# Performance work log

Measured on AMD Instinct MI355X. Metric: run time of the kernel, lower is better.

Reference implementation:

```python
import jax, jax.numpy as jnp
import numpy as np

H = 1024

def setup_inputs() -> dict:
    key = jax.random.key(0)
    k1, k2, k3, k4, k5 = jax.random.split(key, 5)
    B, T = 32, 2048
    s = 1.0 / np.sqrt(H)
    return {
        "decoder_state": jax.random.normal(k1, (B, H), dtype=jnp.float32),
        "encoder_states": jax.random.normal(k2, (B, T, H), dtype=jnp.float32),
        "Wa_w": jax.random.uniform(k3, (H, H), jnp.float32, -s, s),
        "Wa_b": jnp.zeros((H,), jnp.float32),
        "Ua_w": jax.random.uniform(k4, (H, H), jnp.float32, -s, s),
        "Ua_b": jnp.zeros((H,), jnp.float32),
        "v_w": jax.random.uniform(k5, (H,), jnp.float32, -s, s),
        "v_b": jnp.zeros((), jnp.float32),
    }

def reference(decoder_state, encoder_states, Wa_w, Wa_b, Ua_w, Ua_b, v_w, v_b):
    # decoder_state: [B,H], encoder_states: [B,T,H]
    dec_proj = decoder_state @ Ua_w.T + Ua_b            # [B,H]
    enc_proj = jnp.einsum('bth,oh->bto', encoder_states, Wa_w) + Wa_b  # [B,T,H]
    e = jnp.tanh(dec_proj[:, None, :] + enc_proj)        # [B,T,H]
    scores = jnp.einsum('bth,h->bt', e, v_w) + v_b       # [B,T]
    attn_weights = jax.nn.softmax(scores, axis=1)        # [B,T]
    context = jnp.einsum('bt,bth->bh', attn_weights, encoder_states)  # [B,H]
    return (context, attn_weights)
```

## Files before the change

kernel.cpp:

```cpp
#include <hip/hip_runtime.h>
#include <hip/hip_bf16.h>

#define HH 1024
#define BB 32
#define TT 2048

typedef __attribute__((ext_vector_type(8))) short bf16x8;
typedef __attribute__((ext_vector_type(4))) float f32x4;

static __device__ __forceinline__ unsigned short f2bf(float f) {
    unsigned int u = __float_as_uint(f);
    unsigned int r = u + 0x7fffu + ((u >> 16) & 1u);
    return (unsigned short)(r >> 16);
}
static __device__ __forceinline__ float bf2f(unsigned short u) {
    return __uint_as_float(((unsigned int)u) << 16);
}
static __device__ __forceinline__ float fast_tanh(float x) {
    float e = __expf(2.0f * x);
    return 1.0f - 2.0f / (e + 1.0f);
}

#define GLOAD_LDS16(gp, lp) \
    __builtin_amdgcn_global_load_lds( \
        (const __attribute__((address_space(1))) void*)(gp), \
        (__attribute__((address_space(3))) void*)(lp), 16, 0, 0)

__global__ void k_convW(const float* __restrict__ W, unsigned short* __restrict__ Wb) {
    int i = blockIdx.x * 256 + threadIdx.x;
    float4 v = ((const float4*)W)[i];
    ushort4 o;
    o.x = f2bf(v.x); o.y = f2bf(v.y); o.z = f2bf(v.z); o.w = f2bf(v.w);
    ((ushort4*)Wb)[i] = o;
}

__global__ void k_convEnc(const float* __restrict__ E, unsigned short* __restrict__ Eb) {
    long i = ((long)blockIdx.x * 256 + threadIdx.x) * 8;
    float4 a = *(const float4*)(E + i);
    float4 b = *(const float4*)(E + i + 4);
    ushort4 o0, o1;
    o0.x = f2bf(a.x); o0.y = f2bf(a.y); o0.z = f2bf(a.z); o0.w = f2bf(a.w);
    o1.x = f2bf(b.x); o1.y = f2bf(b.y); o1.z = f2bf(b.z); o1.w = f2bf(b.w);
    *(ushort4*)(Eb + i) = o0;
    *(ushort4*)(Eb + i + 4) = o1;
}

__global__ void k_decproj(const float* __restrict__ dec, const float* __restrict__ Ua,
                          const float* __restrict__ Uab, const float* __restrict__ Wab,
                          float* __restrict__ dp) {
    int gtid = blockIdx.x * 256 + threadIdx.x;
    int b = gtid >> 10, o = gtid & 1023;
    const float4* d4 = (const float4*)(dec + (long)b * HH);
    const float4* u4 = (const float4*)(Ua + (long)o * HH);
    float acc = 0.f;
    for (int k = 0; k < HH / 4; ++k) {
        float4 a = d4[k], w = u4[k];
        acc += a.x * w.x + a.y * w.y + a.z * w.z + a.w * w.w;
    }
    dp[gtid] = acc + Uab[o] + Wab[o];
}

__global__ __launch_bounds__(512) void k_score_bf(
        const unsigned short* __restrict__ encb, const unsigned short* __restrict__ Wb,
        const float* __restrict__ dp, const float* __restrict__ vw,
        float* __restrict__ scores) {
    __shared__ __align__(16) unsigned short As[2][256 * 64];
    __shared__ __align__(16) unsigned short Bs[2][256 * 64];
    int bid = blockIdx.x;
    int xcd = bid & 7;
    int ord = bid >> 3;
    int nt = ord & 3;
    int mt = (ord >> 2) * 8 + xcd;
    long m0 = (long)mt * 256;
    int o0b = nt * 256;
    int tid = threadIdx.x;
    int lane = tid & 63, wid = tid >> 6;
    int wm = wid >> 2, wn = wid & 3;
    int r = lane & 15, g = lane >> 4;

    f32x4 acc[8][4];
    #pragma unroll
    for (int i = 0; i < 8; ++i)
        #pragma unroll
        for (int j = 0; j < 4; ++j) acc[i][j] = (f32x4){0.f, 0.f, 0.f, 0.f};

    int srow = tid >> 3;
    int swu = (tid & 7) ^ (srow & 7);
    const unsigned short* aSrc = encb + (m0 + srow) * HH + swu * 8;
    const unsigned short* bSrc = Wb + (long)(o0b + srow) * HH + swu * 8;
    int ldso = wid * 512;
    int rx = r & 7;
    int u0 = (g ^ rx) * 8;
    int u1 = ((4 + g) ^ rx) * 8;

    auto stage = [&](int bi, int kc) {
        #pragma unroll
        for (int p = 0; p < 4; ++p)
            GLOAD_LDS16(aSrc + kc + p * 64 * HH, &As[bi][ldso + p * 4096]);
        #pragma unroll
        for (int p = 0; p < 4; ++p)
            GLOAD_LDS16(bSrc + kc + p * 64 * HH, &Bs[bi][ldso + p * 4096]);
    };

    auto compute = [&](int bi) {
        bf16x8 bfr[4][2];
        #pragma unroll
        for (int ni = 0; ni < 4; ++ni) {
            int rowb = (wn * 64 + ni * 16 + r) * 64;
            bfr[ni][0] = *(const bf16x8*)(&Bs[bi][rowb + u0]);
            bfr[ni][1] = *(const bf16x8*)(&Bs[bi][rowb + u1]);
        }
        __builtin_amdgcn_s_setprio(1);
        #pragma unroll
        for (int mi = 0; mi < 8; ++mi) {
            int rowa = (wm * 128 + mi * 16 + r) * 64;
            bf16x8 a0 = *(const bf16x8*)(&As[bi][rowa + u0]);
            bf16x8 a1 = *(const bf16x8*)(&As[bi][rowa + u1]);
            #pragma unroll
            for (int ni = 0; ni < 4; ++ni) {
                acc[mi][ni] = __builtin_amdgcn_mfma_f32_16x16x32_bf16(
                    a0, bfr[ni][0], acc[mi][ni], 0, 0, 0);
                acc[mi][ni] = __builtin_amdgcn_mfma_f32_16x16x32_bf16(
                    a1, bfr[ni][1], acc[mi][ni], 0, 0, 0);
            }
        }
        __builtin_amdgcn_s_setprio(0);
    };

    stage(0, 0);
    stage(1, 64);
    asm volatile("s_waitcnt vmcnt(8)" ::: "memory");
    __builtin_amdgcn_s_barrier();

    #pragma unroll 1
    for (int t = 0; t < 16; ++t) {
        compute(t & 1);
        if (t == 15) break;
        __builtin_amdgcn_s_barrier();
        if (t < 14) {
            stage(t & 1, (t + 2) * 64);
            asm volatile("s_waitcnt vmcnt(8)" ::: "memory");
        } else {
            asm volatile("s_waitcnt vmcnt(0)" ::: "memory");
        }
        __builtin_amdgcn_s_barrier();
    }

    int bb = (int)(m0 >> 11);
    float vv[4], dpv[4];
    #pragma unroll
    for (int ni = 0; ni < 4; ++ni) {
        int o = o0b + wn * 64 + ni * 16 + r;
        vv[ni] = vw[o];
        dpv[ni] = dp[bb * HH + o];
    }
    #pragma unroll
    for (int mi = 0; mi < 8; ++mi) {
        float vp[4] = {0.f, 0.f, 0.f, 0.f};
        #pragma unroll
        for (int ni = 0; ni < 4; ++ni)
            #pragma unroll
            for (int j = 0; j < 4; ++j)
                vp[j] += fast_tanh(acc[mi][ni][j] + dpv[ni]) * vv[ni];
        #pragma unroll
        for (int j = 0; j < 4; ++j) {
            float s = vp[j];
            s += __shfl_xor(s, 1); s += __shfl_xor(s, 2);
            s += __shfl_xor(s, 4); s += __shfl_xor(s, 8);
            if (r == 0) {
                int row = wm * 128 + mi * 16 + g * 4 + j;
                atomicAdd(&scores[m0 + row], s);
            }
        }
    }
}

#define LDSP 40
__global__ __launch_bounds__(256) void k_score(const float* __restrict__ enc,
        const unsigned short* __restrict__ Wb, const float* __restrict__ dp,
        const float* __restrict__ vw, float* __restrict__ scores) {
    __shared__ __align__(16) unsigned short As[128][LDSP];
    __shared__ __align__(16) unsigned short Bs[128][LDSP];
    int bid = blockIdx.x;
    int nt = bid & 7;
    int mt = bid >> 3;
    long m0 = (long)mt * 128;
    int o0 = nt * 128;
    int tid = threadIdx.x;
    int lane = tid & 63, wid = tid >> 6;
    int wm = wid >> 1, wn = wid & 1;
    int r = lane & 15, g = lane >> 4;

    f32x4 acc[4][4];
    #pragma unroll
    for (int i = 0; i < 4; ++i)
        #pragma unroll
        for (int j = 0; j < 4; ++j) acc[i][j] = (f32x4){0.f, 0.f, 0.f, 0.f};

    for (int kc = 0; kc < HH; kc += 32) {
        #pragma unroll
        for (int i = 0; i < 4; ++i) {
            int idx = tid + i * 256;
            int row = idx >> 3, kq = idx & 7;
            float4 a = *(const float4*)(enc + (m0 + row) * HH + kc + kq * 4);
            ushort4 p;
            p.x = f2bf(a.x); p.y = f2bf(a.y); p.z = f2bf(a.z); p.w = f2bf(a.w);
            *(ushort4*)(&As[row][kq * 4]) = p;
        }
        #pragma unroll
        for (int i = 0; i < 2; ++i) {
            int idx = tid + i * 256;
            int row = idx >> 2, kq = idx & 3;
            *(int4*)(&Bs[row][kq * 8]) =
                *(const int4*)(Wb + (long)(o0 + row) * HH + kc + kq * 8);
        }
        __syncthreads();
        bf16x8 af[4], bfr[4];
        #pragma unroll
        for (int mi = 0; mi < 4; ++mi)
            af[mi] = *(const bf16x8*)(&As[wm * 64 + mi * 16 + r][g * 8]);
        #pragma unroll
        for (int ni = 0; ni < 4; ++ni)
            bfr[ni] = *(const bf16x8*)(&Bs[wn * 64 + ni * 16 + r][g * 8]);
        #pragma unroll
        for (int mi = 0; mi < 4; ++mi)
            #pragma unroll
            for (int ni = 0; ni < 4; ++ni)
                acc[mi][ni] = __builtin_amdgcn_mfma_f32_16x16x32_bf16(
                    af[mi], bfr[ni], acc[mi][ni], 0, 0, 0);
        __syncthreads();
    }

    int bb = (int)(m0 >> 11);
    #pragma unroll
    for (int mi = 0; mi < 4; ++mi) {
        float vp[4] = {0.f, 0.f, 0.f, 0.f};
        #pragma unroll
        for (int ni = 0; ni < 4; ++ni) {
            int o = o0 + wn * 64 + ni * 16 + r;
            float vvs = vw[o];
            float dpvs = dp[bb * HH + o];
            #pragma unroll
            for (int j = 0; j < 4; ++j)
                vp[j] += fast_tanh(acc[mi][ni][j] + dpvs) * vvs;
        }
        #pragma unroll
        for (int j = 0; j < 4; ++j) {
            float s = vp[j];
            s += __shfl_xor(s, 1); s += __shfl_xor(s, 2);
            s += __shfl_xor(s, 4); s += __shfl_xor(s, 8);
            if (r == 0) {
                int row = wm * 64 + mi * 16 + g * 4 + j;
                atomicAdd(&scores[m0 + row], s);
            }
        }
    }
}

__global__ void k_softmax(float* __restrict__ w) {
    int b = blockIdx.x;
    float* row = w + (long)b * TT;
    int tid = threadIdx.x;
    float loc[8];
    float m = -1e30f;
    #pragma unroll
    for (int i = 0; i < 8; ++i) { loc[i] = row[tid + i * 256]; m = fmaxf(m, loc[i]); }
    #pragma unroll
    for (int off = 1; off < 64; off <<= 1) m = fmaxf(m, __shfl_xor(m, off));
    __shared__ float red[4];
    if ((tid & 63) == 0) red[tid >> 6] = m;
    __syncthreads();
    m = fmaxf(fmaxf(red[0], red[1]), fmaxf(red[2], red[3]));
    float s = 0.f;
    #pragma unroll
    for (int i = 0; i < 8; ++i) { loc[i] = __expf(loc[i] - m); s += loc[i]; }
    #pragma unroll
    for (int off = 1; off < 64; off <<= 1) s += __shfl_xor(s, off);
    __shared__ float red2[4];
    if ((tid & 63) == 0) red2[tid >> 6] = s;
    __syncthreads();
    s = red2[0] + red2[1] + red2[2] + red2[3];
    float inv = 1.0f / s;
    #pragma unroll
    for (int i = 0; i < 8; ++i) row[tid + i * 256] = loc[i] * inv;
}

__global__ void k_context_bf(const unsigned short* __restrict__ encb,
                             const float* __restrict__ w, float* __restrict__ ctx) {
    int bid = blockIdx.x;
    int b = bid >> 4;
    int ts = bid & 15;
    int h = threadIdx.x * 4;
    const float* wr = w + (long)b * TT + ts * 128;
    long base = ((long)b * TT + (long)ts * 128) * HH + h;
    float a0 = 0.f, a1 = 0.f, a2 = 0.f, a3 = 0.f;
    #pragma unroll 4
    for (int t = 0; t < 128; ++t) {
        ushort4 e = *(const ushort4*)(encb + base + (long)t * HH);
        float ww = wr[t];
        a0 += ww * bf2f(e.x);
        a1 += ww * bf2f(e.y);
        a2 += ww * bf2f(e.z);
        a3 += ww * bf2f(e.w);
    }
    atomicAdd(&ctx[b * HH + h], a0);
    atomicAdd(&ctx[b * HH + h + 1], a1);
    atomicAdd(&ctx[b * HH + h + 2], a2);
    atomicAdd(&ctx[b * HH + h + 3], a3);
}

__global__ void k_context(const float* __restrict__ enc, const float* __restrict__ w,
                          float* __restrict__ ctx) {
    int bid = blockIdx.x;
    int b = bid >> 6;
    int hc = (bid >> 4) & 3;
    int ts = bid & 15;
    int h = hc * 256 + threadIdx.x;
    const float* wr = w + (long)b * TT + ts * 128;
    long base = ((long)b * TT + (long)ts * 128) * HH + h;
    float acc = 0.f;
    for (int t = 0; t < 128; ++t)
        acc += wr[t] * enc[base + (long)t * HH];
    atomicAdd(&ctx[b * HH + h], acc);
}

extern "C" void kernel_launch(void* const* d_in, const int* in_sizes, int n_in,
                              void* d_out, int out_size, void* d_ws, size_t ws_size,
                              hipStream_t stream) {
    const float* dec  = (const float*)d_in[0];
    const float* enc  = (const float*)d_in[1];
    const float* Wa_w = (const float*)d_in[2];
    const float* Wa_b = (const float*)d_in[3];
    const float* Ua_w = (const float*)d_in[4];
    const float* Ua_b = (const float*)d_in[5];
    const float* v_w  = (const float*)d_in[6];

    float* out  = (float*)d_out;
    float* ctx  = out;
    float* attn = out + BB * HH;

    float* dpw = (float*)d_ws;
    unsigned short* Wb = (unsigned short*)((char*)d_ws + 131072);
    unsigned short* encb = (unsigned short*)((char*)d_ws + 131072 + 2097152);
    const size_t NEED = 131072ull + 2097152ull + (size_t)BB * TT * HH * 2;

    hipMemsetAsync(d_out, 0, (size_t)out_size * sizeof(float), stream);
    k_convW<<<1024, 256, 0, stream>>>(Wa_w, Wb);
    k_decproj<<<128, 256, 0, stream>>>(dec, Ua_w, Ua_b, Wa_b, dpw);

    if (ws_size >= NEED) {
        k_convEnc<<<32768, 256, 0, stream>>>(enc, encb);
        k_score_bf<<<1024, 512, 0, stream>>>(encb, Wb, dpw, v_w, attn);
        k_softmax<<<BB, 256, 0, stream>>>(attn);
        k_context_bf<<<512, 256, 0, stream>>>(encb, attn, ctx);
    } else {
        k_score<<<4096, 256, 0, stream>>>(enc, Wb, dpw, v_w, attn);
        k_softmax<<<BB, 256, 0, stream>>>(attn);
        k_context<<<2048, 256, 0, stream>>>(enc, attn, ctx);
    }
}
```

Before: 310.4 us.

## Interleave next-tile global-to-LDS prefetch with MFMA compute in GEMM main loop

Restructures the double-buffered GEMM loop so the global-to-LDS loads for the next K chunk are issued in pieces between groups of MFMAs, instead of a separate stage step between two barriers. A-fragment LDS reads are also double-buffered in registers so the next rows load while the current MFMAs run. Prefetch depth drops from two tiles ahead to one, with a single __syncthreads per iteration in place of two barriers plus explicit vmcnt waits. The aim is better overlap of memory and matrix work, at the cost of a shallower prefetch and a full sync that drains all outstanding loads each iteration.

```diff
diff --git a/kernel.cpp b/kernel.cpp
--- a/kernel.cpp
+++ b/kernel.cpp
@@ -93,16 +93,19 @@
     int u0 = (g ^ rx) * 8;
     int u1 = ((4 + g) ^ rx) * 8;
 
-    auto stage = [&](int bi, int kc) {
-        #pragma unroll
-        for (int p = 0; p < 4; ++p)
-            GLOAD_LDS16(aSrc + kc + p * 64 * HH, &As[bi][ldso + p * 4096]);
-        #pragma unroll
-        for (int p = 0; p < 4; ++p)
-            GLOAD_LDS16(bSrc + kc + p * 64 * HH, &Bs[bi][ldso + p * 4096]);
-    };
-
-    auto compute = [&](int bi) {
+    #pragma unroll
+    for (int p = 0; p < 4; ++p) {
+        GLOAD_LDS16(aSrc + p * 64 * HH, &As[0][ldso + p * 4096]);
+        GLOAD_LDS16(bSrc + p * 64 * HH, &Bs[0][ldso + p * 4096]);
+    }
+    __syncthreads();
+
+    #pragma unroll 1
+    for (int t = 0; t < 16; ++t) {
+        int bi = t & 1, pi = bi ^ 1;
+        int kc2 = (t + 1) * 64;
+        bool pre = (t < 15);
+
         bf16x8 bfr[4][2];
         #pragma unroll
         for (int ni = 0; ni < 4; ++ni) {
@@ -110,40 +113,49 @@
             bfr[ni][0] = *(const bf16x8*)(&Bs[bi][rowb + u0]);
             bfr[ni][1] = *(const bf16x8*)(&Bs[bi][rowb + u1]);
         }
-        __builtin_amdgcn_s_setprio(1);
-        #pragma unroll
-        for (int mi = 0; mi < 8; ++mi) {
-            int rowa = (wm * 128 + mi * 16 + r) * 64;
-            bf16x8 a0 = *(const bf16x8*)(&As[bi][rowa + u0]);
-            bf16x8 a1 = *(const bf16x8*)(&As[bi][rowa + u1]);
+        bf16x8 aq[2][2][2];
+        #pragma unroll
+        for (int q = 0; q < 2; ++q) {
+            int rowa = (wm * 128 + q * 16 + r) * 64;
+            aq[0][q][0] = *(const bf16x8*)(&As[bi][rowa + u0]);
+            aq[0][q][1] = *(const bf16x8*)(&As[bi][rowa + u1]);
+        }
+
+        #pragma unroll
+        for (int p = 0; p < 4; ++p) {
+            if (pre && p < 2) {
+                GLOAD_LDS16(aSrc + kc2 + (2 * p) * 64 * HH,
+                            &As[pi][ldso + (2 * p) * 4096]);
+                GLOAD_LDS16(aSrc + kc2 + (2 * p + 1) * 64 * HH,
+                            &As[pi][ldso + (2 * p + 1) * 4096]);
+                GLOAD_LDS16(bSrc + kc2 + (2 * p) * 64 * HH,
+                            &Bs[pi][ldso + (2 * p) * 4096]);
+                GLOAD_LDS16(bSrc + kc2 + (2 * p + 1) * 64 * HH,
+                            &Bs[pi][ldso + (2 * p + 1) * 4096]);
+            }
+            if (p < 3) {
+                #pragma unroll
+                for (int q = 0; q < 2; ++q) {
+                    int rowa = (wm * 128 + (2 * (p + 1) + q) * 16 + r) * 64;
+                    aq[(p + 1) & 1][q][0] = *(const bf16x8*)(&As[bi][rowa + u0]);
+                    aq[(p + 1) & 1][q][1] = *(const bf16x8*)(&As[bi][rowa + u1]);
+                }
+            }
+            __builtin_amdgcn_s_setprio(1);
             #pragma unroll
-            for (int ni = 0; ni < 4; ++ni) {
-                acc[mi][ni] = __builtin_amdgcn_mfma_f32_16x16x32_bf16(
-                    a0, bfr[ni][0], acc[mi][ni], 0, 0, 0);
-                acc[mi][ni] = __builtin_amdgcn_mfma_f32_16x16x32_bf16(
-                    a1, bfr[ni][1], acc[mi][ni], 0, 0, 0);
-            }
-        }
-        __builtin_amdgcn_s_setprio(0);
-    };
-
-    stage(0, 0);
-    stage(1, 64);
-    asm volatile("s_waitcnt vmcnt(8)" ::: "memory");
-    __builtin_amdgcn_s_barrier();
-
-    #pragma unroll 1
-    for (int t = 0; t < 16; ++t) {
-        compute(t & 1);
-        if (t == 15) break;
-        __builtin_amdgcn_s_barrier();
-        if (t < 14) {
-            stage(t & 1, (t + 2) * 64);
-            asm volatile("s_waitcnt vmcnt(8)" ::: "memory");
-        } else {
-            asm volatile("s_waitcnt vmcnt(0)" ::: "memory");
-        }
-        __builtin_amdgcn_s_barrier();
+            for (int q = 0; q < 2; ++q) {
+                int mi = 2 * p + q;
+                #pragma unroll
+                for (int ni = 0; ni < 4; ++ni) {
+                    acc[mi][ni] = __builtin_amdgcn_mfma_f32_16x16x32_bf16(
+                        aq[p & 1][q][0], bfr[ni][0], acc[mi][ni], 0, 0, 0);
+                    acc[mi][ni] = __builtin_amdgcn_mfma_f32_16x16x32_bf16(
+                        aq[p & 1][q][1], bfr[ni][1], acc[mi][ni], 0, 0, 0);
+                }
+            }
+            __builtin_amdgcn_s_setprio(0);
+        }
+        __syncthreads();
     }
 
     int bb = (int)(m0 >> 11);
```

Result: faster. 292.7 us, median of 2 (-5.7%).
